# Performance work log

Hardware: AMD Instinct MI355X
Metric: run time of the kernel (lower is better)

## Reference

```python
import jax, jax.numpy as jnp
import numpy as np

HEADS = 12

def setup_inputs() -> dict:
    key = jax.random.key(0)
    k1, k2, k3 = jax.random.split(key, 3)
    b, n, d = 8, 1024, 768
    x = jax.random.normal(k1, (b, n, d), dtype=jnp.float32)
    # xavier_uniform-like init for linear weights
    lim_qkv = float(np.sqrt(6.0 / (d + 3 * d)))
    W_qkv = jax.random.uniform(k2, (3 * d, d), dtype=jnp.float32, minval=-lim_qkv, maxval=lim_qkv)
    b_qkv = jnp.zeros((3 * d,), dtype=jnp.float32)
    lim_o = float(np.sqrt(6.0 / (d + d)))
    W_out = jax.random.uniform(k3, (d, d), dtype=jnp.float32, minval=-lim_o, maxval=lim_o)
    b_out = jnp.zeros((d,), dtype=jnp.float32)
    return {"x": x, "W_qkv": W_qkv, "b_qkv": b_qkv, "W_out": W_out, "b_out": b_out}

def reference(x, W_qkv, b_qkv, W_out, b_out):
    b, n, d = x.shape
    h = HEADS
    hd = d // h
    scale = d ** (-0.5)  # NOTE: original scales by dim**-0.5, not head_dim**-0.5
    qkv = x @ W_qkv.T + b_qkv                      # [b, n, 3d]
    q, k, v = jnp.split(qkv, 3, axis=-1)           # each [b, n, d]
    def to_heads(t):
        return t.reshape(b, n, h, hd).transpose(0, 2, 1, 3)  # [b, h, n, hd]
    q, k, v = to_heads(q), to_heads(k), to_heads(v)
    dots = jnp.einsum('bhid,bhjd->bhij', q, k) * scale       # [b, h, n, n]
    attn = jax.nn.softmax(dots, axis=-1)
    out = jnp.einsum('bhij,bhjd->bhid', attn, v)             # [b, h, n, hd]
    out = out.transpose(0, 2, 1, 3).reshape(b, n, d)
    return out @ W_out.T + b_out
```

## Files before the change

kernel.cpp:

```cpp
#include <hip/hip_runtime.h>
#include <stdint.h>

typedef __bf16 bf16x8 __attribute__((ext_vector_type(8)));
typedef float  f32x4  __attribute__((ext_vector_type(4)));
typedef unsigned short u16;

#define AS1 __attribute__((address_space(1)))
#define AS3 __attribute__((address_space(3)))
#define G2L(gp, lp) __builtin_amdgcn_global_load_lds( \
    (const AS1 unsigned int*)(uintptr_t)(gp), \
    (AS3 unsigned int*)(uintptr_t)(lp), 16, 0, 0)

static __device__ __forceinline__ u16 f32_to_bf16(float f) {
    unsigned u = __float_as_uint(f);
    u += 0x7fffu + ((u >> 16) & 1u);
    return (u16)(u >> 16);
}

static __device__ __forceinline__ unsigned pack_bf16(float lo, float hi) {
    return (unsigned)f32_to_bf16(lo) | ((unsigned)f32_to_bf16(hi) << 16);
}

static __device__ __forceinline__ float fast_exp2(float x) {
    return __builtin_amdgcn_exp2f(x);
}

static __device__ __forceinline__ f32x4 mfma16(bf16x8 a, bf16x8 b, f32x4 c) {
    return __builtin_amdgcn_mfma_f32_16x16x32_bf16(a, b, c, 0, 0, 0);
}

__global__ void cvt3_k(const float* __restrict__ a, const float* __restrict__ b,
                       const float* __restrict__ c, u16* __restrict__ out) {
    const int i = blockIdx.x * blockDim.x + threadIdx.x;
    const float* src; int off;
    if (i < 1572864)      { src = a; off = 0; }
    else if (i < 2015232) { src = b; off = 1572864; }
    else                  { src = c; off = 2015232; }
    const float4 v = reinterpret_cast<const float4*>(src)[i - off];
    reinterpret_cast<uint2*>(out)[i] = make_uint2(pack_bf16(v.x, v.y), pack_bf16(v.z, v.w));
}

template<int OUTF32>
__global__ __launch_bounds__(256, 2) void gemm_bt_k(const u16* __restrict__ A, const u16* __restrict__ B,
                                                    const float* __restrict__ bias, void* __restrict__ Cp,
                                                    int M, int N, int K, int nbx) {
    __shared__ __align__(16) u16 As[2][128 * 64];
    __shared__ __align__(16) u16 Bs[2][128 * 64];
    const int id = blockIdx.x;
    const int cpx = gridDim.x >> 3;
    const int swz = (id & 7) * cpx + (id >> 3);
    const int bx = swz % nbx, by = swz / nbx;
    const int t = threadIdx.x, w = t >> 6, l = t & 63, lr = l & 15, lg = l >> 4;
    const int wr = w >> 1, wc = w & 1;
    const long rowBase = (long)by * 128;
    const long colBase = (long)bx * 128;

    const f32x4 z = {0.f, 0.f, 0.f, 0.f};
    f32x4 acc[4][4];
    #pragma unroll
    for (int m = 0; m < 4; ++m)
        #pragma unroll
        for (int n = 0; n < 4; ++n) acc[m][n] = z;

    const int kSteps = K >> 6;
    #pragma unroll
    for (int i = 0; i < 4; ++i) {
        const int c = i * 256 + t, row = c >> 3, ch = c & 7;
        const int sch = ch ^ (row & 7);
        G2L(A + (rowBase + row) * K + sch * 8, &As[0][(i * 256 + w * 64) * 8]);
        G2L(B + (colBase + row) * K + sch * 8, &Bs[0][(i * 256 + w * 64) * 8]);
    }
    for (int kt = 0; kt < kSteps; ++kt) {
        const int cur = kt & 1;
        asm volatile("s_waitcnt vmcnt(0)" ::: "memory");
        __builtin_amdgcn_sched_barrier(0);
        __builtin_amdgcn_s_barrier();
        __builtin_amdgcn_sched_barrier(0);
        if (kt + 1 < kSteps) {
            const int k0 = (kt + 1) << 6;
            #pragma unroll
            for (int i = 0; i < 4; ++i) {
                const int c = i * 256 + t, row = c >> 3, ch = c & 7;
                const int sch = ch ^ (row & 7);
                G2L(A + (rowBase + row) * K + k0 + sch * 8, &As[cur ^ 1][(i * 256 + w * 64) * 8]);
                G2L(B + (colBase + row) * K + k0 + sch * 8, &Bs[cur ^ 1][(i * 256 + w * 64) * 8]);
            }
        }
        __builtin_amdgcn_sched_barrier(0);
        #pragma unroll
        for (int kk = 0; kk < 2; ++kk) {
            bf16x8 af[4], bfr[4];
            #pragma unroll
            for (int m = 0; m < 4; ++m) {
                const int row = wr * 64 + m * 16 + lr;
                af[m] = *reinterpret_cast<const bf16x8*>(&As[cur][row * 64 + (((kk * 4 + lg) ^ (lr & 7)) << 3)]);
            }
            #pragma unroll
            for (int n = 0; n < 4; ++n) {
                const int row = wc * 64 + n * 16 + lr;
                bfr[n] = *reinterpret_cast<const bf16x8*>(&Bs[cur][row * 64 + (((kk * 4 + lg) ^ (lr & 7)) << 3)]);
            }
            #pragma unroll
            for (int m = 0; m < 4; ++m)
                #pragma unroll
                for (int n = 0; n < 4; ++n) acc[m][n] = mfma16(af[m], bfr[n], acc[m][n]);
        }
    }
    #pragma unroll
    for (int n = 0; n < 4; ++n) {
        const long gc = colBase + wc * 64 + n * 16 + lr;
        const float bv = bias[gc];
        #pragma unroll
        for (int m = 0; m < 4; ++m) {
            const long gr = rowBase + wr * 64 + m * 16 + lg * 4;
            #pragma unroll
            for (int r = 0; r < 4; ++r) {
                const float v = acc[m][n][r] + bv;
                if (OUTF32) reinterpret_cast<float*>(Cp)[(gr + r) * N + gc] = v;
                else        reinterpret_cast<u16*>(Cp)[(gr + r) * N + gc] = f32_to_bf16(v);
            }
        }
    }
}

__global__ __launch_bounds__(256) void transpose_v_k(const u16* __restrict__ qkv, u16* __restrict__ vt) {
    const int bh = blockIdx.y, b = bh / 12, h = bh % 12;
    const int nt = blockIdx.x;
    __shared__ __align__(16) u16 Ts[64][72];
    const int t = threadIdx.x;
    const int rr = t >> 2;
    #pragma unroll
    for (int i = 0; i < 2; ++i) {
        const int ch = (t & 3) + i * 4;
        const u16* src = qkv + (long)(b * 1024 + nt * 64 + rr) * 2304 + 1536 + h * 64 + ch * 8;
        *reinterpret_cast<uint4*>(&Ts[rr][ch * 8]) = *reinterpret_cast<const uint4*>(src);
    }
    __syncthreads();
    #pragma unroll
    for (int i = 0; i < 2; ++i) {
        const int ch = (t & 3) + i * 4;
        u16 vals[8];
        #pragma unroll
        for (int j = 0; j < 8; ++j)
            vals[j] = Ts[(j & 3) * 16 + ch * 2 + (j >> 2)][rr];
        u16* dst = vt + (long)(bh * 64 + rr) * 1024 + nt * 64 + ch * 8;
        *reinterpret_cast<uint4*>(dst) = *reinterpret_cast<const uint4*>(vals);
    }
}

__global__ __launch_bounds__(256, 4) void attn_k(const u16* __restrict__ qkv, const u16* __restrict__ vt,
                                                 u16* __restrict__ outp) {
    const int id = blockIdx.x;
    const int bh = id % 96, qt = id / 96;
    const int b = bh / 12, h = bh % 12;
    const int t = threadIdx.x, w = t >> 6, l = t & 63, lr = l & 15, lg = l >> 4;
    __shared__ __align__(16) u16 Ks[2][64 * 64];
    __shared__ __align__(16) u16 Vts[2][64 * 64];
    __shared__ __align__(16) u16 Ps[4 * 16 * 64];

    const u16* kb = qkv + 768 + h * 64;
    const u16* vb = vt + (long)bh * 64 * 1024;

    #pragma unroll
    for (int i = 0; i < 2; ++i) {
        const int c = (i * 4 + w) * 64 + l;
        const int row = c >> 3, sch = (c & 7) ^ (row & 7);
        G2L(kb + (long)(b * 1024 + row) * 2304 + sch * 8, &Ks[0][(i * 4 + w) * 512]);
        G2L(vb + (long)row * 1024 + sch * 8, &Vts[0][(i * 4 + w) * 512]);
    }
    #pragma unroll
    for (int j = 0; j < 2; ++j) {
        const int c = j * 256 + t, row = c >> 3, ch = c & 7;
        const uint4 q = *reinterpret_cast<const uint4*>(
            qkv + (long)(b * 1024 + qt * 64 + row) * 2304 + h * 64 + ch * 8);
        *reinterpret_cast<uint4*>(&Ps[row * 64 + ((ch ^ (row & 7)) << 3)]) = q;
    }
    __syncthreads();
    bf16x8 aq[2];
    #pragma unroll
    for (int kk = 0; kk < 2; ++kk)
        aq[kk] = *reinterpret_cast<const bf16x8*>(&Ps[(w * 16 + lr) * 64 + (((kk * 4 + lg) ^ (lr & 7)) << 3)]);

    const f32x4 z = {0.f, 0.f, 0.f, 0.f};
    f32x4 o[4] = {z, z, z, z};
    float lacc[4] = {0.f, 0.f, 0.f, 0.f};
    const float sc2 = 0.052058773f;

    for (int kt = 0; kt < 16; ++kt) {
        const int cur = kt & 1;
        asm volatile("s_waitcnt vmcnt(0)" ::: "memory");
        __builtin_amdgcn_sched_barrier(0);
        __builtin_amdgcn_s_barrier();
        __builtin_amdgcn_sched_barrier(0);
        if (kt < 15) {
            const int ktn = kt + 1;
            #pragma unroll
            for (int i = 0; i < 2; ++i) {
                const int c = (i * 4 + w) * 64 + l;
                const int row = c >> 3, sch = (c & 7) ^ (row & 7);
                G2L(kb + (long)(b * 1024 + ktn * 64 + row) * 2304 + sch * 8, &Ks[cur ^ 1][(i * 4 + w) * 512]);
                G2L(vb + (long)row * 1024 + ktn * 64 + sch * 8, &Vts[cur ^ 1][(i * 4 + w) * 512]);
            }
        }
        __builtin_amdgcn_sched_barrier(0);
        f32x4 s[4] = {z, z, z, z};
        #pragma unroll
        for (int kk = 0; kk < 2; ++kk) {
            #pragma unroll
            for (int kc = 0; kc < 4; ++kc) {
                const int row = kc * 16 + lr;
                bf16x8 bk = *reinterpret_cast<const bf16x8*>(&Ks[cur][row * 64 + (((kk * 4 + lg) ^ (lr & 7)) << 3)]);
                s[kc] = mfma16(aq[kk], bk, s[kc]);
            }
        }
        #pragma unroll
        for (int r = 0; r < 4; ++r) {
            const float p0 = fast_exp2(s[0][r] * sc2);
            const float p1 = fast_exp2(s[1][r] * sc2);
            const float p2 = fast_exp2(s[2][r] * sc2);
            const float p3 = fast_exp2(s[3][r] * sc2);
            lacc[r] += (p0 + p1) + (p2 + p3);
            const unsigned w0 = pack_bf16(p0, p1);
            const unsigned w1 = pack_bf16(p2, p3);
            const int q = lg * 4 + r;
            const int csw = (lr >> 1) ^ (q & 7);
            *reinterpret_cast<uint2*>(&Ps[w * 1024 + q * 64 + csw * 8 + (lr & 1) * 4]) = make_uint2(w0, w1);
        }
        #pragma unroll
        for (int kk = 0; kk < 2; ++kk) {
            bf16x8 pa = *reinterpret_cast<const bf16x8*>(&Ps[w * 1024 + lr * 64 + (((kk * 4 + lg) ^ (lr & 7)) << 3)]);
            #pragma unroll
            for (int n = 0; n < 4; ++n) {
                const int row = n * 16 + lr;
                bf16x8 vbf = *reinterpret_cast<const bf16x8*>(&Vts[cur][row * 64 + (((kk * 4 + lg) ^ (lr & 7)) << 3)]);
                o[n] = mfma16(pa, vbf, o[n]);
            }
        }
    }
    #pragma unroll
    for (int r = 0; r < 4; ++r) {
        float rs = lacc[r];
        #pragma unroll
        for (int off = 1; off < 16; off <<= 1) rs += __shfl_xor(rs, off, 64);
        lacc[r] = rs;
    }
    const int qrow = qt * 64 + w * 16 + lg * 4;
    #pragma unroll
    for (int n = 0; n < 4; ++n) {
        #pragma unroll
        for (int r = 0; r < 4; ++r) {
            const float v = o[n][r] / lacc[r];
            outp[(long)(b * 1024 + qrow + r) * 768 + h * 64 + n * 16 + lr] = f32_to_bf16(v);
        }
    }
}

extern "C" void kernel_launch(void* const* d_in, const int* in_sizes, int n_in,
                              void* d_out, int out_size, void* d_ws, size_t ws_size,
                              hipStream_t stream) {
    (void)in_sizes; (void)n_in; (void)out_size; (void)ws_size;
    const float* x    = (const float*)d_in[0];
    const float* Wqkv = (const float*)d_in[1];
    const float* bqkv = (const float*)d_in[2];
    const float* Wout = (const float*)d_in[3];
    const float* bout = (const float*)d_in[4];

    u16* xb   = (u16*)d_ws;
    u16* Wqb  = xb  + 6291456;
    u16* Wob  = Wqb + 1769472;
    u16* qkv  = Wob + 589824;
    u16* vtb  = qkv + 18874368;
    u16* attn = vtb + 6291456;

    cvt3_k<<<8448, 256, 0, stream>>>(x, Wqkv, Wout, xb);

    gemm_bt_k<0><<<1152, 256, 0, stream>>>(xb, Wqb, bqkv, qkv, 8192, 2304, 768, 18);
    transpose_v_k<<<dim3(16, 96), 256, 0, stream>>>(qkv, vtb);
    attn_k<<<1536, 256, 0, stream>>>(qkv, vtb, attn);
    gemm_bt_k<1><<<384, 256, 0, stream>>>(attn, Wob, bout, d_out, 8192, 768, 768, 6);
}
```

Baseline: 116.1 us.

## Process two query tiles per attention block to reuse K/V tiles

Each attention block now handles 128 query rows, as two 64-row groups per wave, instead of 64, and the grid is halved. Every K and V tile loaded into shared memory therefore feeds twice as many MFMAs, which halves global K/V traffic and per-tile barrier overhead. The cost is doubled register use for accumulators and scores, larger shared memory for P, and lower occupancy (launch bounds 4 to 3). With 768 blocks there are also fewer blocks to spread across the CUs.

Measured after the change: 114.4 us. Within noise of the previous version (-1.4%).

```diff
diff --git a/kernel.cpp b/kernel.cpp
--- a/kernel.cpp
+++ b/kernel.cpp
@@ -148,7 +148,7 @@
     }
 }
 
-__global__ __launch_bounds__(256, 4) void attn_k(const u16* __restrict__ qkv, const u16* __restrict__ vt,
+__global__ __launch_bounds__(256, 3) void attn_k(const u16* __restrict__ qkv, const u16* __restrict__ vt,
                                                  u16* __restrict__ outp) {
     const int id = blockIdx.x;
     const int bh = id % 96, qt = id / 96;
@@ -156,7 +156,7 @@
     const int t = threadIdx.x, w = t >> 6, l = t & 63, lr = l & 15, lg = l >> 4;
     __shared__ __align__(16) u16 Ks[2][64 * 64];
     __shared__ __align__(16) u16 Vts[2][64 * 64];
-    __shared__ __align__(16) u16 Ps[4 * 16 * 64];
+    __shared__ __align__(16) u16 Ps[8192];
 
     const u16* kb = qkv + 768 + h * 64;
     const u16* vb = vt + (long)bh * 64 * 1024;
@@ -169,21 +169,28 @@
         G2L(vb + (long)row * 1024 + sch * 8, &Vts[0][(i * 4 + w) * 512]);
     }
     #pragma unroll
-    for (int j = 0; j < 2; ++j) {
+    for (int j = 0; j < 4; ++j) {
         const int c = j * 256 + t, row = c >> 3, ch = c & 7;
         const uint4 q = *reinterpret_cast<const uint4*>(
-            qkv + (long)(b * 1024 + qt * 64 + row) * 2304 + h * 64 + ch * 8);
+            qkv + (long)(b * 1024 + qt * 128 + row) * 2304 + h * 64 + ch * 8);
         *reinterpret_cast<uint4*>(&Ps[row * 64 + ((ch ^ (row & 7)) << 3)]) = q;
     }
     __syncthreads();
-    bf16x8 aq[2];
-    #pragma unroll
-    for (int kk = 0; kk < 2; ++kk)
-        aq[kk] = *reinterpret_cast<const bf16x8*>(&Ps[(w * 16 + lr) * 64 + (((kk * 4 + lg) ^ (lr & 7)) << 3)]);
+    bf16x8 aq[2][2];
+    #pragma unroll
+    for (int qg = 0; qg < 2; ++qg)
+        #pragma unroll
+        for (int kk = 0; kk < 2; ++kk)
+            aq[qg][kk] = *reinterpret_cast<const bf16x8*>(
+                &Ps[(qg * 64 + w * 16 + lr) * 64 + (((kk * 4 + lg) ^ (lr & 7)) << 3)]);
 
     const f32x4 z = {0.f, 0.f, 0.f, 0.f};
-    f32x4 o[4] = {z, z, z, z};
-    float lacc[4] = {0.f, 0.f, 0.f, 0.f};
+    f32x4 o[2][4];
+    #pragma unroll
+    for (int qg = 0; qg < 2; ++qg)
+        #pragma unroll
+        for (int n = 0; n < 4; ++n) o[qg][n] = z;
+    float lacc[2][4] = {{0.f, 0.f, 0.f, 0.f}, {0.f, 0.f, 0.f, 0.f}};
     const float sc2 = 0.052058773f;
 
     for (int kt = 0; kt < 16; ++kt) {
@@ -203,54 +210,69 @@
             }
         }
         __builtin_amdgcn_sched_barrier(0);
-        f32x4 s[4] = {z, z, z, z};
+        f32x4 s[2][4];
+        #pragma unroll
+        for (int qg = 0; qg < 2; ++qg)
+            #pragma unroll
+            for (int kc = 0; kc < 4; ++kc) s[qg][kc] = z;
         #pragma unroll
         for (int kk = 0; kk < 2; ++kk) {
             #pragma unroll
             for (int kc = 0; kc < 4; ++kc) {
                 const int row = kc * 16 + lr;
                 bf16x8 bk = *reinterpret_cast<const bf16x8*>(&Ks[cur][row * 64 + (((kk * 4 + lg) ^ (lr & 7)) << 3)]);
-                s[kc] = mfma16(aq[kk], bk, s[kc]);
-            }
-        }
-        #pragma unroll
-        for (int r = 0; r < 4; ++r) {
-            const float p0 = fast_exp2(s[0][r] * sc2);
-            const float p1 = fast_exp2(s[1][r] * sc2);
-            const float p2 = fast_exp2(s[2][r] * sc2);
-            const float p3 = fast_exp2(s[3][r] * sc2);
-            lacc[r] += (p0 + p1) + (p2 + p3);
-            const unsigned w0 = pack_bf16(p0, p1);
-            const unsigned w1 = pack_bf16(p2, p3);
-            const int q = lg * 4 + r;
-            const int csw = (lr >> 1) ^ (q & 7);
-            *reinterpret_cast<uint2*>(&Ps[w * 1024 + q * 64 + csw * 8 + (lr & 1) * 4]) = make_uint2(w0, w1);
+                s[0][kc] = mfma16(aq[0][kk], bk, s[0][kc]);
+                s[1][kc] = mfma16(aq[1][kk], bk, s[1][kc]);
+            }
+        }
+        #pragma unroll
+        for (int qg = 0; qg < 2; ++qg) {
+            #pragma unroll
+            for (int r = 0; r < 4; ++r) {
+                const float p0 = fast_exp2(s[qg][0][r] * sc2);
+                const float p1 = fast_exp2(s[qg][1][r] * sc2);
+                const float p2 = fast_exp2(s[qg][2][r] * sc2);
+                const float p3 = fast_exp2(s[qg][3][r] * sc2);
+                lacc[qg][r] += (p0 + p1) + (p2 + p3);
+                const unsigned w0 = pack_bf16(p0, p1);
+                const unsigned w1 = pack_bf16(p2, p3);
+                const int q = lg * 4 + r;
+                const int csw = (lr >> 1) ^ (q & 7);
+                *reinterpret_cast<uint2*>(&Ps[w * 2048 + qg * 1024 + q * 64 + csw * 8 + (lr & 1) * 4]) =
+                    make_uint2(w0, w1);
+            }
         }
         #pragma unroll
         for (int kk = 0; kk < 2; ++kk) {
-            bf16x8 pa = *reinterpret_cast<const bf16x8*>(&Ps[w * 1024 + lr * 64 + (((kk * 4 + lg) ^ (lr & 7)) << 3)]);
+            const int swzk = ((kk * 4 + lg) ^ (lr & 7)) << 3;
+            bf16x8 pa0 = *reinterpret_cast<const bf16x8*>(&Ps[w * 2048 + lr * 64 + swzk]);
+            bf16x8 pa1 = *reinterpret_cast<const bf16x8*>(&Ps[w * 2048 + 1024 + lr * 64 + swzk]);
             #pragma unroll
             for (int n = 0; n < 4; ++n) {
                 const int row = n * 16 + lr;
-                bf16x8 vbf = *reinterpret_cast<const bf16x8*>(&Vts[cur][row * 64 + (((kk * 4 + lg) ^ (lr & 7)) << 3)]);
-                o[n] = mfma16(pa, vbf, o[n]);
-            }
-        }
-    }
-    #pragma unroll
-    for (int r = 0; r < 4; ++r) {
-        float rs = lacc[r];
-        #pragma unroll
-        for (int off = 1; off < 16; off <<= 1) rs += __shfl_xor(rs, off, 64);
-        lacc[r] = rs;
-    }
-    const int qrow = qt * 64 + w * 16 + lg * 4;
-    #pragma unroll
-    for (int n = 0; n < 4; ++n) {
+                bf16x8 vbf = *reinterpret_cast<const bf16x8*>(&Vts[cur][row * 64 + swzk]);
+                o[0][n] = mfma16(pa0, vbf, o[0][n]);
+                o[1][n] = mfma16(pa1, vbf, o[1][n]);
+            }
+        }
+    }
+    #pragma unroll
+    for (int qg = 0; qg < 2; ++qg) {
         #pragma unroll
         for (int r = 0; r < 4; ++r) {
-            const float v = o[n][r] / lacc[r];
-            outp[(long)(b * 1024 + qrow + r) * 768 + h * 64 + n * 16 + lr] = f32_to_bf16(v);
+            float rs = lacc[qg][r];
+            #pragma unroll
+            for (int off = 1; off < 16; off <<= 1) rs += __shfl_xor(rs, off, 64);
+            lacc[qg][r] = rs;
+        }
+        const int qrow = qt * 128 + qg * 64 + w * 16 + lg * 4;
+        #pragma unroll
+        for (int n = 0; n < 4; ++n) {
+            #pragma unroll
+            for (int r = 0; r < 4; ++r) {
+                const float v = o[qg][n][r] / lacc[qg][r];
+                outp[(long)(b * 1024 + qrow + r) * 768 + h * 64 + n * 16 + lr] = f32_to_bf16(v);
+            }
         }
     }
 }
@@ -276,6 +298,6 @@
 
     gemm_bt_k<0><<<1152, 256, 0, stream>>>(xb, Wqb, bqkv, qkv, 8192, 2304, 768, 18);
     transpose_v_k<<<dim3(16, 96), 256, 0, stream>>>(qkv, vtb);
-    attn_k<<<1536, 256, 0, stream>>>(qkv, vtb, attn);
+    attn_k<<<768, 256, 0, stream>>>(qkv, vtb, attn);
     gemm_bt_k<1><<<384, 256, 0, stream>>>(attn, Wob, bout, d_out, 8192, 768, 768, 6);
 }
```
